# Optimization experiments

Measured on AMD Instinct MI355X. Metric: run time of the kernel, lower is better.

## Reference

```python
import jax, jax.numpy as jnp
import numpy as np

N = 50000
E = 800000
D_IN = 128
D_HID = 512
D_OUT = 128
BN_EPS = 1e-5


def setup_inputs() -> dict:
    key = jax.random.key(0)
    ks = jax.random.split(key, 12)
    inp = {}
    inp["v"] = jax.random.normal(ks[0], (N, D_IN), dtype=jnp.float32)
    inp["src"] = jax.random.randint(ks[1], (E,), 0, N, dtype=jnp.int32)
    inp["dst"] = jax.random.randint(ks[2], (E,), 0, N, dtype=jnp.int32)
    inp["edge_weight"] = jax.random.uniform(ks[3], (E,), dtype=jnp.float32)
    # learned parameters
    inp["epsilon"] = jnp.zeros((1, 1), dtype=jnp.float32)  # nn.Parameter([[0.0]])
    s1 = 1.0 / np.sqrt(D_IN)
    s2 = 1.0 / np.sqrt(D_HID)
    inp["W1"] = jax.random.uniform(ks[4], (D_IN, D_HID), minval=-s1, maxval=s1, dtype=jnp.float32)
    inp["b1"] = jax.random.uniform(ks[5], (D_HID,), minval=-s1, maxval=s1, dtype=jnp.float32)
    inp["gamma1"] = jnp.ones((D_HID,), dtype=jnp.float32)
    inp["beta1"] = jnp.zeros((D_HID,), dtype=jnp.float32)
    inp["W2"] = jax.random.uniform(ks[6], (D_HID, D_OUT), minval=-s2, maxval=s2, dtype=jnp.float32)
    inp["b2"] = jax.random.uniform(ks[7], (D_OUT,), minval=-s2, maxval=s2, dtype=jnp.float32)
    inp["gamma2"] = jnp.ones((D_OUT,), dtype=jnp.float32)
    inp["beta2"] = jnp.zeros((D_OUT,), dtype=jnp.float32)
    return inp


def _batchnorm(x, gamma, beta):
    # training-mode BN: batch mean / biased variance over the node axis
    mean = jnp.mean(x, axis=0)
    var = jnp.mean(jnp.square(x - mean), axis=0)
    return gamma * (x - mean) * jax.lax.rsqrt(var + BN_EPS) + beta


def reference(v, src, dst, edge_weight, epsilon, W1, b1, gamma1, beta1, W2, b2, gamma2, beta2):
    n = v.shape[0]
    # sparse.mm(a, v): out[dst] += w * v[src]
    msgs = v[src] * edge_weight[:, None]               # [E, D_IN]
    v_agg = jax.ops.segment_sum(msgs, dst, num_segments=n)  # [N, D_IN]
    v_agg = v_agg + epsilon * v                        # epsilon residual
    h = jax.nn.relu(_batchnorm(v_agg @ W1 + b1, gamma1, beta1))
    out = jax.nn.relu(_batchnorm(h @ W2 + b2, gamma2, beta2))
    return out
```

## Files before the change

kernel.cpp:

```cpp
#include <hip/hip_runtime.h>

#define N_NODES 50000
#define E_EDGES 800000
#define D_INF   128
#define D_HIDF  512
#define D_OUTF  128
#define SCAN_NB ((N_NODES + 255) / 256)
#define M1BLKS  ((N_NODES + 255) / 256)
#define FBLKS   ((N_NODES + 63) / 64)
#define EQ      (E_EDGES / 4)

#define CAST_NB  3125
#define PREPW_NB 256
#define HIST_NB  ((EQ + 255) / 256)
#define PREP_ALL_NB (CAST_NB + 2 * PREPW_NB + HIST_NB)

typedef unsigned short u16;
typedef __attribute__((ext_vector_type(8))) short short8;
typedef __attribute__((ext_vector_type(4))) float floatx4;
typedef const __attribute__((address_space(1))) void gas_t;
typedef __attribute__((address_space(3))) void las_t;

__device__ __forceinline__ u16 f2bf(float f) {
    union { float f; unsigned u; } v; v.f = f;
    unsigned r = (v.u + 0x7fffu + ((v.u >> 16) & 1u)) >> 16;
    return (u16)r;
}
__device__ __forceinline__ float bf2f(u16 b) {
    union { unsigned u; float f; } v; v.u = ((unsigned)b) << 16; return v.f;
}

__global__ __launch_bounds__(256) void prep_all_kernel(
        const float* __restrict__ v, const float* __restrict__ W1,
        const float* __restrict__ W2, const int* __restrict__ dst,
        u16* __restrict__ vbf, u16* __restrict__ W1t, u16* __restrict__ W2t,
        int* __restrict__ counts, int* __restrict__ pos) {
    int b = blockIdx.x;
    int tid = threadIdx.x;
    if (b < CAST_NB) {
        int i = b * 256 + tid;
        const float4 a = ((const float4*)v)[i * 2];
        const float4 c = ((const float4*)v)[i * 2 + 1];
        u16 o[8];
        o[0] = f2bf(a.x); o[1] = f2bf(a.y); o[2] = f2bf(a.z); o[3] = f2bf(a.w);
        o[4] = f2bf(c.x); o[5] = f2bf(c.y); o[6] = f2bf(c.z); o[7] = f2bf(c.w);
        ((float4*)vbf)[i] = *(const float4*)o;
    } else if (b < CAST_NB + PREPW_NB) {
        int idx = (b - CAST_NB) * 256 + tid;
        int k1 = idx >> 9, n1 = idx & 511;
        W1t[n1 * 128 + k1] = f2bf(W1[idx]);
    } else if (b < CAST_NB + 2 * PREPW_NB) {
        int idx = (b - CAST_NB - PREPW_NB) * 256 + tid;
        int k2 = idx >> 7, n2 = idx & 127;
        W2t[n2 * 512 + k2] = f2bf(W2[idx]);
    } else {
        int t = (b - CAST_NB - 2 * PREPW_NB) * 256 + tid;
        if (t >= EQ) return;
        int d0 = dst[t];
        int d1 = dst[t + EQ];
        int d2 = dst[t + 2 * EQ];
        int d3 = dst[t + 3 * EQ];
        int p0 = atomicAdd(&counts[d0], 1);
        int p1 = atomicAdd(&counts[d1], 1);
        int p2 = atomicAdd(&counts[d2], 1);
        int p3 = atomicAdd(&counts[d3], 1);
        pos[t]          = p0;
        pos[t + EQ]     = p1;
        pos[t + 2 * EQ] = p2;
        pos[t + 3 * EQ] = p3;
    }
}

__global__ __launch_bounds__(256) void reduce_kernel(const int* __restrict__ counts,
                                                     int* __restrict__ block_sums) {
    __shared__ int lsum[4];
    int tid = threadIdx.x;
    int gid = blockIdx.x * 256 + tid;
    int s = (gid < N_NODES) ? counts[gid] : 0;
#pragma unroll
    for (int off = 32; off; off >>= 1) s += __shfl_down(s, off);
    if ((tid & 63) == 0) lsum[tid >> 6] = s;
    __syncthreads();
    if (tid == 0) block_sums[blockIdx.x] = lsum[0] + lsum[1] + lsum[2] + lsum[3];
}

__global__ __launch_bounds__(256) void scan_final(const int* __restrict__ counts,
                                                  const int* __restrict__ block_sums,
                                                  int* __restrict__ row_start) {
    __shared__ int sh[256];
    __shared__ int bs[256];
    int tid = threadIdx.x;
    int gid = blockIdx.x * 256 + tid;
    sh[tid] = (gid < N_NODES) ? counts[gid] : 0;
    bs[tid] = (tid < SCAN_NB) ? block_sums[tid] : 0;
    __syncthreads();
    for (int off = 1; off < 256; off <<= 1) {
        int t1 = (tid >= off) ? sh[tid - off] : 0;
        int t2 = (tid >= off) ? bs[tid - off] : 0;
        __syncthreads();
        sh[tid] += t1;
        bs[tid] += t2;
        __syncthreads();
    }
    int boff = (blockIdx.x == 0) ? 0 : bs[blockIdx.x - 1];
    int excl = (tid == 0) ? 0 : sh[tid - 1];
    if (gid < N_NODES) row_start[gid] = boff + excl;
    if (gid == 0) row_start[N_NODES] = E_EDGES;
}

__global__ void fill_kernel(const int* __restrict__ src, const int* __restrict__ dst,
                            const float* __restrict__ w, const int* __restrict__ pos,
                            const int* __restrict__ row_start,
                            int2* __restrict__ csr_ew) {
    int e = blockIdx.x * blockDim.x + threadIdx.x;
    if (e >= E_EDGES) return;
    int d = dst[e];
    int idx = row_start[d] + pos[e];
    int2 rec;
    rec.x = src[e];
    rec.y = __float_as_int(w[e]);
    csr_ew[idx] = rec;
}

__global__ __launch_bounds__(256) void gather_kernel(const u16* __restrict__ vbf,
                                                     const int* __restrict__ row_start,
                                                     const int2* __restrict__ csr_ew,
                                                     const float* __restrict__ eps_p,
                                                     u16* __restrict__ vagg) {
    int node = blockIdx.x * 16 + (threadIdx.x >> 4);
    if (node >= N_NODES) return;
    int c8 = (threadIdx.x & 15) << 3;
    int beg = row_start[node];
    int end = row_start[node + 1];
    float a[8] = {};
    int j = beg;
    for (; j + 1 < end; j += 2) {
        int2 e0 = csr_ew[j];
        int2 e1 = csr_ew[j + 1];
        float w0 = __int_as_float(e0.y);
        float w1 = __int_as_float(e1.y);
        float4 r0 = *(const float4*)(vbf + (size_t)e0.x * D_INF + c8);
        float4 r1 = *(const float4*)(vbf + (size_t)e1.x * D_INF + c8);
        const u16* p0 = (const u16*)&r0;
        const u16* p1 = (const u16*)&r1;
#pragma unroll
        for (int t = 0; t < 8; ++t) a[t] += w0 * bf2f(p0[t]);
#pragma unroll
        for (int t = 0; t < 8; ++t) a[t] += w1 * bf2f(p1[t]);
    }
    if (j < end) {
        int2 e0 = csr_ew[j];
        float w0 = __int_as_float(e0.y);
        float4 r0 = *(const float4*)(vbf + (size_t)e0.x * D_INF + c8);
        const u16* p0 = (const u16*)&r0;
#pragma unroll
        for (int t = 0; t < 8; ++t) a[t] += w0 * bf2f(p0[t]);
    }
    float e = eps_p[0];
    float4 rn = *(const float4*)(vbf + (size_t)node * D_INF + c8);
    const u16* pn = (const u16*)&rn;
    u16 o[8];
#pragma unroll
    for (int t = 0; t < 8; ++t) o[t] = f2bf(a[t] + e * bf2f(pn[t]));
    *(float4*)(vagg + (size_t)node * D_INF + c8) = *(const float4*)o;
}

__global__ __launch_bounds__(512) void stats_gemm1(
        const u16* __restrict__ A, const u16* __restrict__ Bt,
        const float* __restrict__ bias,
        float* __restrict__ psum, float* __restrict__ psq, int M) {
    __shared__ __align__(16) char smem[24576];
    u16* As = (u16*)smem;
    u16* Bs = (u16*)(smem + 16384);
    const int bm = blockIdx.y * 256;
    const int bn = blockIdx.x * 128;
    const int tid = threadIdx.x;
    const int wave = tid >> 6, lane = tid & 63;
    const int wr = wave >> 1, wc = wave & 1;
    const int wm = wr * 64, wn = wc * 64;
    const int lm = lane & 15, quad = lane >> 4;
    floatx4 acc[4][4] = {};
    for (int ks = 0; ks < 4; ++ks) {
        const int k0 = ks << 5;
        {
            const int sub = lane >> 2, s = lane & 3;
#pragma unroll
            for (int t = 0; t < 3; ++t) {
                int ch = wave * 3 + t;
                if (ch < 16) {
                    int row = ch * 16 + sub;
                    int grow = bm + row; if (grow > M - 1) grow = M - 1;
                    int ss = s ^ (row & 3);
                    __builtin_amdgcn_global_load_lds(
                        (gas_t*)(A + (size_t)grow * 128 + k0 + ss * 8),
                        (las_t*)(As + row * 32 + s * 8), 16, 0, 0);
                } else {
                    int row = (ch - 16) * 16 + sub;
                    int ss = s ^ (row & 3);
                    __builtin_amdgcn_global_load_lds(
                        (gas_t*)(Bt + (size_t)(bn + row) * 128 + k0 + ss * 8),
                        (las_t*)(Bs + row * 32 + s * 8), 16, 0, 0);
                }
            }
        }
        __syncthreads();
        short8 af[4], bfr[4];
#pragma unroll
        for (int i = 0; i < 4; ++i) {
            int row = wm + i * 16 + lm;
            af[i] = *(const short8*)&As[row * 32 + ((quad ^ (row & 3)) * 8)];
        }
#pragma unroll
        for (int j = 0; j < 4; ++j) {
            int row = wn + j * 16 + lm;
            bfr[j] = *(const short8*)&Bs[row * 32 + ((quad ^ (row & 3)) * 8)];
        }
#pragma unroll
        for (int i = 0; i < 4; ++i)
#pragma unroll
            for (int j = 0; j < 4; ++j)
                acc[i][j] = __builtin_amdgcn_mfma_f32_16x16x32_bf16(af[i], bfr[j], acc[i][j], 0, 0, 0);
        __syncthreads();
    }
    float* redS = (float*)smem;
    float* redQ = redS + 128;
    if (tid < 128) { redS[tid] = 0.f; redQ[tid] = 0.f; }
    __syncthreads();
#pragma unroll
    for (int j = 0; j < 4; ++j) {
        int cl = wn + j * 16 + lm;
        float bj = bias[bn + cl];
        float s = 0.f, q = 0.f;
#pragma unroll
        for (int i = 0; i < 4; ++i) {
            int row0 = bm + wm + i * 16 + quad * 4;
#pragma unroll
            for (int r = 0; r < 4; ++r)
                if (row0 + r < M) { float x = acc[i][j][r] + bj; s += x; q += x * x; }
        }
        s += __shfl_xor(s, 16); q += __shfl_xor(q, 16);
        s += __shfl_xor(s, 32); q += __shfl_xor(q, 32);
        if (quad == 0) { atomicAdd(&redS[cl], s); atomicAdd(&redQ[cl], q); }
    }
    __syncthreads();
    if (tid < 128) {
        psum[(size_t)blockIdx.y * 512 + bn + tid] = redS[tid];
        psq [(size_t)blockIdx.y * 512 + bn + tid] = redQ[tid];
    }
}

__global__ __launch_bounds__(512, 4) void fused_mlp(
        const u16* __restrict__ vagg, const u16* __restrict__ W1t,
        const u16* __restrict__ W2t,
        const float* __restrict__ b1, const float* __restrict__ scale1,
        const float* __restrict__ shift1, const float* __restrict__ b2,
        u16* __restrict__ x2, float* __restrict__ psum, float* __restrict__ psq,
        int M) {
    __shared__ __align__(16) char smem[81920];
    u16* As  = (u16*)smem;
    u16* W1s = (u16*)(smem + 16384);
    u16* W2s = (u16*)smem;
    u16* hs  = (u16*)(smem + 16384);
    const int bm = blockIdx.x * 64;
    const int tid = threadIdx.x;
    const int wave = tid >> 6, lane = tid & 63;
    const int wr = wave >> 2, wc = wave & 3;
    const int wm = wr * 32;
    const int wn1 = wc * 128;
    const int wn2 = wc * 32;
    const int lm = lane & 15, quad = lane >> 4;

    floatx4 acc1[2][8] = {};
    floatx4 acc2[2][2] = {};

    auto stage_w1 = [&](int win) {
#pragma unroll
        for (int u = 0; u < 8; ++u) {
            int c = tid + u * 512;
            int col = c >> 3, s = c & 7;
            __builtin_amdgcn_global_load_lds(
                (gas_t*)(W1t + (size_t)col * 128 + win * 64 + ((s ^ (col & 7)) * 8)),
                (las_t*)(W1s + col * 64 + s * 8), 16, 0, 0);
        }
    };
    auto stage_w2 = [&](int win) {
#pragma unroll
        for (int u = 0; u < 2; ++u) {
            int c = tid + u * 512;
            int n = c >> 3, s = c & 7;
            __builtin_amdgcn_global_load_lds(
                (gas_t*)(W2t + (size_t)n * 512 + win * 64 + ((s ^ (n & 7)) * 8)),
                (las_t*)(W2s + n * 64 + s * 8), 16, 0, 0);
        }
    };
    auto compute1 = [&](int ks) {
        short8 a[2], b[8];
#pragma unroll
        for (int i = 0; i < 2; ++i) {
            int row = wm + i * 16 + lm;
            a[i] = *(const short8*)&As[row * 128 + (((ks * 4 + quad) ^ (row & 7)) * 8)];
        }
#pragma unroll
        for (int j = 0; j < 8; ++j) {
            int col = wn1 + j * 16 + lm;
            b[j] = *(const short8*)&W1s[col * 64 + ((((ks & 1) * 4 + quad) ^ (col & 7)) * 8)];
        }
#pragma unroll
        for (int i = 0; i < 2; ++i)
#pragma unroll
            for (int j = 0; j < 8; ++j)
                acc1[i][j] = __builtin_amdgcn_mfma_f32_16x16x32_bf16(a[i], b[j], acc1[i][j], 0, 0, 0);
    };
    auto compute2 = [&](int ks) {
        short8 a[2], b[2];
#pragma unroll
        for (int i = 0; i < 2; ++i) {
            int row = wm + i * 16 + lm;
            a[i] = *(const short8*)&hs[row * 512 + (((ks * 4 + quad) ^ (row & 7)) * 8)];
        }
#pragma unroll
        for (int j = 0; j < 2; ++j) {
            int n = wn2 + j * 16 + lm;
            b[j] = *(const short8*)&W2s[n * 64 + ((((ks & 1) * 4 + quad) ^ (n & 7)) * 8)];
        }
#pragma unroll
        for (int i = 0; i < 2; ++i)
#pragma unroll
            for (int j = 0; j < 2; ++j)
                acc2[i][j] = __builtin_amdgcn_mfma_f32_16x16x32_bf16(a[i], b[j], acc2[i][j], 0, 0, 0);
    };

#pragma unroll
    for (int u = 0; u < 2; ++u) {
        int c = tid + u * 512;
        int row = c >> 4, s = c & 15;
        int grow = bm + row; if (grow > M - 1) grow = M - 1;
        __builtin_amdgcn_global_load_lds(
            (gas_t*)(vagg + (size_t)grow * 128 + ((s ^ (row & 7)) * 8)),
            (las_t*)(As + row * 128 + s * 8), 16, 0, 0);
    }
    stage_w1(0);
    __syncthreads();
    compute1(0); compute1(1);
    __syncthreads();
    stage_w1(1);
    __syncthreads();
    compute1(2); compute1(3);
    __syncthreads();

    stage_w2(0);
    {
        float hsc[8], hsh[8];
#pragma unroll
        for (int j = 0; j < 8; ++j) {
            int col = wn1 + j * 16 + lm;
            float sc = scale1[col];
            hsc[j] = sc;
            hsh[j] = shift1[col] + sc * b1[col];
        }
#pragma unroll
        for (int i = 0; i < 2; ++i)
#pragma unroll
            for (int j = 0; j < 8; ++j)
#pragma unroll
                for (int r = 0; r < 4; ++r) {
                    int row = wm + i * 16 + quad * 4 + r;
                    int col = wn1 + j * 16 + lm;
                    float hv = fmaxf(0.f, acc1[i][j][r] * hsc[j] + hsh[j]);
                    hs[row * 512 + (((col >> 3) ^ (row & 7)) * 8) + (col & 7)] = f2bf(hv);
                }
    }
    __syncthreads();

#pragma unroll
    for (int win = 0; win < 8; ++win) {
        compute2(win * 2); compute2(win * 2 + 1);
        __syncthreads();
        if (win < 7) { stage_w2(win + 1); __syncthreads(); }
    }

    float* redS = (float*)smem;
    float* redQ = redS + 128;
    if (tid < 128) { redS[tid] = 0.f; redQ[tid] = 0.f; }
    __syncthreads();
    float bj2[2];
#pragma unroll
    for (int j = 0; j < 2; ++j) {
        int cl = wn2 + j * 16 + lm;
        bj2[j] = b2[cl];
        float s = 0.f, q = 0.f;
#pragma unroll
        for (int i = 0; i < 2; ++i) {
            int row0 = bm + wm + i * 16 + quad * 4;
#pragma unroll
            for (int r = 0; r < 4; ++r)
                if (row0 + r < M) { float x = acc2[i][j][r] + bj2[j]; s += x; q += x * x; }
        }
        s += __shfl_xor(s, 16); q += __shfl_xor(q, 16);
        s += __shfl_xor(s, 32); q += __shfl_xor(q, 32);
        if (quad == 0) { atomicAdd(&redS[cl], s); atomicAdd(&redQ[cl], q); }
    }
    __syncthreads();
    if (tid < 128) {
        psum[(size_t)blockIdx.x * 128 + tid] = redS[tid];
        psq [(size_t)blockIdx.x * 128 + tid] = redQ[tid];
    }
    __syncthreads();

    float* obuf = (float*)smem;
#pragma unroll
    for (int i = 0; i < 2; ++i)
#pragma unroll
        for (int j = 0; j < 2; ++j)
#pragma unroll
            for (int r = 0; r < 4; ++r) {
                int row = wm + i * 16 + quad * 4 + r;
                int col = wn2 + j * 16 + lm;
                obuf[row * 132 + col] = acc2[i][j][r] + bj2[j];
            }
    __syncthreads();
    {
        int row = tid >> 3, seg = (tid & 7) * 16;
        int grow = bm + row;
        if (grow < M) {
            u16 ob[16];
#pragma unroll
            for (int t = 0; t < 4; ++t) {
                float4 f = *(float4*)&obuf[row * 132 + seg + t * 4];
                ob[t * 4 + 0] = f2bf(f.x);
                ob[t * 4 + 1] = f2bf(f.y);
                ob[t * 4 + 2] = f2bf(f.z);
                ob[t * 4 + 3] = f2bf(f.w);
            }
            u16* dp = x2 + (size_t)grow * 128 + seg;
            *(float4*)dp       = *(float4*)ob;
            *(float4*)(dp + 8) = *(float4*)(ob + 8);
        }
    }
}

__global__ __launch_bounds__(1024) void bn_finalize_kernel(
        const float* __restrict__ psum, const float* __restrict__ psq,
        const float* __restrict__ gamma, const float* __restrict__ beta,
        float* __restrict__ scale, float* __restrict__ shift,
        int nblocks, int Ncols, float inv_n) {
    __shared__ float shS[16][64];
    __shared__ float shQ[16][64];
    const int tx = threadIdx.x;
    const int ty = threadIdx.y;
    const int c = blockIdx.x * 64 + tx;
    float s = 0.f, q = 0.f;
    for (int b = ty; b < nblocks; b += 16) {
        s += psum[(size_t)b * Ncols + c];
        q += psq [(size_t)b * Ncols + c];
    }
    shS[ty][tx] = s;
    shQ[ty][tx] = q;
    __syncthreads();
    if (ty == 0) {
        float S = 0.f, Q = 0.f;
#pragma unroll
        for (int r = 0; r < 16; ++r) { S += shS[r][tx]; Q += shQ[r][tx]; }
        float m = S * inv_n;
        float var = Q * inv_n - m * m;
        float rs = rsqrtf(var + 1e-5f);
        float sc = gamma[c] * rs;
        scale[c] = sc;
        shift[c] = beta[c] - sc * m;
    }
}

__global__ void bn2_apply_kernel(const u16* __restrict__ X, float* __restrict__ Y,
                                 const float* __restrict__ scale,
                                 const float* __restrict__ shift, int n8) {
    int i = blockIdx.x * blockDim.x + threadIdx.x;
    if (i >= n8) return;
    int c = (i & 15) << 3;
    float4 raw = ((const float4*)X)[i];
    const u16* xb = (const u16*)&raw;
    float4 sc0 = *(const float4*)(scale + c);
    float4 sc1 = *(const float4*)(scale + c + 4);
    float4 sh0 = *(const float4*)(shift + c);
    float4 sh1 = *(const float4*)(shift + c + 4);
    float4 y0, y1;
    y0.x = fmaxf(0.f, bf2f(xb[0]) * sc0.x + sh0.x);
    y0.y = fmaxf(0.f, bf2f(xb[1]) * sc0.y + sh0.y);
    y0.z = fmaxf(0.f, bf2f(xb[2]) * sc0.z + sh0.z);
    y0.w = fmaxf(0.f, bf2f(xb[3]) * sc0.w + sh0.w);
    y1.x = fmaxf(0.f, bf2f(xb[4]) * sc1.x + sh1.x);
    y1.y = fmaxf(0.f, bf2f(xb[5]) * sc1.y + sh1.y);
    y1.z = fmaxf(0.f, bf2f(xb[6]) * sc1.z + sh1.z);
    y1.w = fmaxf(0.f, bf2f(xb[7]) * sc1.w + sh1.w);
    ((float4*)Y)[i * 2]     = y0;
    ((float4*)Y)[i * 2 + 1] = y1;
}

extern "C" void kernel_launch(void* const* d_in, const int* in_sizes, int n_in,
                              void* d_out, int out_size, void* d_ws, size_t ws_size,
                              hipStream_t stream) {
    const float* v    = (const float*)d_in[0];
    const int* src    = (const int*)d_in[1];
    const int* dst    = (const int*)d_in[2];
    const float* ew   = (const float*)d_in[3];
    const float* eps  = (const float*)d_in[4];
    const float* W1   = (const float*)d_in[5];
    const float* b1   = (const float*)d_in[6];
    const float* g1   = (const float*)d_in[7];
    const float* be1  = (const float*)d_in[8];
    const float* W2   = (const float*)d_in[9];
    const float* b2   = (const float*)d_in[10];
    const float* g2   = (const float*)d_in[11];
    const float* be2  = (const float*)d_in[12];
    float* out = (float*)d_out;

    char* base = (char*)d_ws;
    u16* vbf  = (u16*)(base + 51200000ull);
    u16* vagg = (u16*)(base + 64000000ull);
    u16* x2   = (u16*)(base + 76800000ull);
    u16* W1t  = (u16*)(base + 89600000ull);
    u16* W2t  = (u16*)(base + 89731072ull);
    float* psum   = (float*)(base + 89862144ull);
    float* psq    = (float*)(base + 90663168ull);
    float* scale1 = (float*)(base + 91464192ull);
    float* shift1 = scale1 + 512;
    float* scale2 = shift1 + 512;
    float* shift2 = scale2 + 128;
    int* counts     = (int*)(shift2 + 128);
    int* row_start  = counts + 50000;
    int* pos        = row_start + 50004;
    int2* csr_ew    = (int2*)(pos + 800000);
    int* block_sums = (int*)(csr_ew + 800000);

    hipMemsetAsync(counts, 0, (size_t)50000 * sizeof(int), stream);

    prep_all_kernel<<<PREP_ALL_NB, 256, 0, stream>>>(v, W1, W2, dst, vbf, W1t, W2t,
                                                     counts, pos);
    reduce_kernel<<<SCAN_NB, 256, 0, stream>>>(counts, block_sums);
    scan_final<<<SCAN_NB, 256, 0, stream>>>(counts, block_sums, row_start);
    fill_kernel<<<(E_EDGES + 255) / 256, 256, 0, stream>>>(src, dst, ew, pos, row_start, csr_ew);
    gather_kernel<<<(N_NODES + 15) / 16, 256, 0, stream>>>(vbf, row_start, csr_ew, eps, vagg);

    {
        dim3 grid(D_HIDF / 128, M1BLKS);
        stats_gemm1<<<grid, 512, 0, stream>>>(vagg, W1t, b1, psum, psq, N_NODES);
    }
    bn_finalize_kernel<<<D_HIDF / 64, dim3(64, 16), 0, stream>>>(
        psum, psq, g1, be1, scale1, shift1, M1BLKS, D_HIDF, 1.0f / N_NODES);

    fused_mlp<<<FBLKS, 512, 0, stream>>>(vagg, W1t, W2t, b1, scale1, shift1, b2,
                                         x2, psum, psq, N_NODES);
    bn_finalize_kernel<<<D_OUTF / 64, dim3(64, 16), 0, stream>>>(
        psum, psq, g2, be2, scale2, shift2, FBLKS, D_OUTF, 1.0f / N_NODES);

    {
        int n8 = N_NODES * D_OUTF / 8;
        bn2_apply_kernel<<<(n8 + 255) / 256, 256, 0, stream>>>(x2, out, scale2, shift2, n8);
    }
}
```

Before: 275.4 us.

## Retile BN1 stats GEMM to full-width rows and widen histogram and gather unrolls

Replaces the 256x128-tiled stats GEMM with a 64-row block kernel that computes all 512 hidden columns per block, mirroring fused_mlp's tiling. A-tile loads are shared across all columns, and partial-stat buffers are placed in dead CSR scratch (pos/csr_ew). The histogram part of the prep kernel now handles 8 edges per thread and runs first, and the gather loop unrolls by 4 edges to keep more loads in flight. This trades more per-block partial sums for BN finalize (782 vs 196 rows) and higher register pressure for better reuse and memory-level parallelism.

```diff
diff --git a/kernel.cpp b/kernel.cpp
--- a/kernel.cpp
+++ b/kernel.cpp
@@ -6,14 +6,13 @@
 #define D_HIDF  512
 #define D_OUTF  128
 #define SCAN_NB ((N_NODES + 255) / 256)
-#define M1BLKS  ((N_NODES + 255) / 256)
 #define FBLKS   ((N_NODES + 63) / 64)
-#define EQ      (E_EDGES / 4)
-
+#define EQ8     (E_EDGES / 8)
+
+#define HIST_NB  ((EQ8 + 255) / 256)
 #define CAST_NB  3125
 #define PREPW_NB 256
-#define HIST_NB  ((EQ + 255) / 256)
-#define PREP_ALL_NB (CAST_NB + 2 * PREPW_NB + HIST_NB)
+#define PREP_ALL_NB (HIST_NB + CAST_NB + 2 * PREPW_NB)
 
 typedef unsigned short u16;
 typedef __attribute__((ext_vector_type(8))) short short8;
@@ -37,37 +36,32 @@
         int* __restrict__ counts, int* __restrict__ pos) {
     int b = blockIdx.x;
     int tid = threadIdx.x;
-    if (b < CAST_NB) {
-        int i = b * 256 + tid;
+    if (b < HIST_NB) {
+        int t = b * 256 + tid;
+        if (t >= EQ8) return;
+        int d[8], p[8];
+#pragma unroll
+        for (int k = 0; k < 8; ++k) d[k] = dst[t + k * EQ8];
+#pragma unroll
+        for (int k = 0; k < 8; ++k) p[k] = atomicAdd(&counts[d[k]], 1);
+#pragma unroll
+        for (int k = 0; k < 8; ++k) pos[t + k * EQ8] = p[k];
+    } else if (b < HIST_NB + CAST_NB) {
+        int i = (b - HIST_NB) * 256 + tid;
         const float4 a = ((const float4*)v)[i * 2];
         const float4 c = ((const float4*)v)[i * 2 + 1];
         u16 o[8];
         o[0] = f2bf(a.x); o[1] = f2bf(a.y); o[2] = f2bf(a.z); o[3] = f2bf(a.w);
         o[4] = f2bf(c.x); o[5] = f2bf(c.y); o[6] = f2bf(c.z); o[7] = f2bf(c.w);
         ((float4*)vbf)[i] = *(const float4*)o;
-    } else if (b < CAST_NB + PREPW_NB) {
-        int idx = (b - CAST_NB) * 256 + tid;
+    } else if (b < HIST_NB + CAST_NB + PREPW_NB) {
+        int idx = (b - HIST_NB - CAST_NB) * 256 + tid;
         int k1 = idx >> 9, n1 = idx & 511;
         W1t[n1 * 128 + k1] = f2bf(W1[idx]);
-    } else if (b < CAST_NB + 2 * PREPW_NB) {
-        int idx = (b - CAST_NB - PREPW_NB) * 256 + tid;
+    } else {
+        int idx = (b - HIST_NB - CAST_NB - PREPW_NB) * 256 + tid;
         int k2 = idx >> 7, n2 = idx & 127;
         W2t[n2 * 512 + k2] = f2bf(W2[idx]);
-    } else {
-        int t = (b - CAST_NB - 2 * PREPW_NB) * 256 + tid;
-        if (t >= EQ) return;
-        int d0 = dst[t];
-        int d1 = dst[t + EQ];
-        int d2 = dst[t + 2 * EQ];
-        int d3 = dst[t + 3 * EQ];
-        int p0 = atomicAdd(&counts[d0], 1);
-        int p1 = atomicAdd(&counts[d1], 1);
-        int p2 = atomicAdd(&counts[d2], 1);
-        int p3 = atomicAdd(&counts[d3], 1);
-        pos[t]          = p0;
-        pos[t + EQ]     = p1;
-        pos[t + 2 * EQ] = p2;
-        pos[t + 3 * EQ] = p3;
     }
 }
 
@@ -134,21 +128,33 @@
     int end = row_start[node + 1];
     float a[8] = {};
     int j = beg;
-    for (; j + 1 < end; j += 2) {
+    for (; j + 3 < end; j += 4) {
         int2 e0 = csr_ew[j];
         int2 e1 = csr_ew[j + 1];
+        int2 e2 = csr_ew[j + 2];
+        int2 e3 = csr_ew[j + 3];
         float w0 = __int_as_float(e0.y);
         float w1 = __int_as_float(e1.y);
+        float w2 = __int_as_float(e2.y);
+        float w3 = __int_as_float(e3.y);
         float4 r0 = *(const float4*)(vbf + (size_t)e0.x * D_INF + c8);
         float4 r1 = *(const float4*)(vbf + (size_t)e1.x * D_INF + c8);
+        float4 r2 = *(const float4*)(vbf + (size_t)e2.x * D_INF + c8);
+        float4 r3 = *(const float4*)(vbf + (size_t)e3.x * D_INF + c8);
         const u16* p0 = (const u16*)&r0;
         const u16* p1 = (const u16*)&r1;
+        const u16* p2 = (const u16*)&r2;
+        const u16* p3 = (const u16*)&r3;
 #pragma unroll
         for (int t = 0; t < 8; ++t) a[t] += w0 * bf2f(p0[t]);
 #pragma unroll
         for (int t = 0; t < 8; ++t) a[t] += w1 * bf2f(p1[t]);
-    }
-    if (j < end) {
+#pragma unroll
+        for (int t = 0; t < 8; ++t) a[t] += w2 * bf2f(p2[t]);
+#pragma unroll
+        for (int t = 0; t < 8; ++t) a[t] += w3 * bf2f(p3[t]);
+    }
+    for (; j < end; ++j) {
         int2 e0 = csr_ew[j];
         float w0 = __int_as_float(e0.y);
         float4 r0 = *(const float4*)(vbf + (size_t)e0.x * D_INF + c8);
@@ -165,88 +171,93 @@
     *(float4*)(vagg + (size_t)node * D_INF + c8) = *(const float4*)o;
 }
 
-__global__ __launch_bounds__(512) void stats_gemm1(
-        const u16* __restrict__ A, const u16* __restrict__ Bt,
-        const float* __restrict__ bias,
+__global__ __launch_bounds__(512, 4) void stats_mlp1(
+        const u16* __restrict__ vagg, const u16* __restrict__ W1t,
+        const float* __restrict__ b1,
         float* __restrict__ psum, float* __restrict__ psq, int M) {
-    __shared__ __align__(16) char smem[24576];
-    u16* As = (u16*)smem;
-    u16* Bs = (u16*)(smem + 16384);
-    const int bm = blockIdx.y * 256;
-    const int bn = blockIdx.x * 128;
+    __shared__ __align__(16) char smem[81920];
+    u16* As  = (u16*)smem;
+    u16* W1s = (u16*)(smem + 16384);
+    const int bm = blockIdx.x * 64;
     const int tid = threadIdx.x;
     const int wave = tid >> 6, lane = tid & 63;
-    const int wr = wave >> 1, wc = wave & 1;
-    const int wm = wr * 64, wn = wc * 64;
+    const int wr = wave >> 2, wc = wave & 3;
+    const int wm = wr * 32;
+    const int wn1 = wc * 128;
     const int lm = lane & 15, quad = lane >> 4;
-    floatx4 acc[4][4] = {};
-    for (int ks = 0; ks < 4; ++ks) {
-        const int k0 = ks << 5;
-        {
-            const int sub = lane >> 2, s = lane & 3;
-#pragma unroll
-            for (int t = 0; t < 3; ++t) {
-                int ch = wave * 3 + t;
-                if (ch < 16) {
-                    int row = ch * 16 + sub;
-                    int grow = bm + row; if (grow > M - 1) grow = M - 1;
-                    int ss = s ^ (row & 3);
-                    __builtin_amdgcn_global_load_lds(
-                        (gas_t*)(A + (size_t)grow * 128 + k0 + ss * 8),
-                        (las_t*)(As + row * 32 + s * 8), 16, 0, 0);
-                } else {
-                    int row = (ch - 16) * 16 + sub;
-                    int ss = s ^ (row & 3);
-                    __builtin_amdgcn_global_load_lds(
-                        (gas_t*)(Bt + (size_t)(bn + row) * 128 + k0 + ss * 8),
-                        (las_t*)(Bs + row * 32 + s * 8), 16, 0, 0);
-                }
-            }
-        }
-        __syncthreads();
-        short8 af[4], bfr[4];
-#pragma unroll
-        for (int i = 0; i < 4; ++i) {
+
+    floatx4 acc1[2][8] = {};
+
+    auto stage_w1 = [&](int win) {
+#pragma unroll
+        for (int u = 0; u < 8; ++u) {
+            int c = tid + u * 512;
+            int col = c >> 3, s = c & 7;
+            __builtin_amdgcn_global_load_lds(
+                (gas_t*)(W1t + (size_t)col * 128 + win * 64 + ((s ^ (col & 7)) * 8)),
+                (las_t*)(W1s + col * 64 + s * 8), 16, 0, 0);
+        }
+    };
+    auto compute1 = [&](int ks) {
+        short8 a[2], b[8];
+#pragma unroll
+        for (int i = 0; i < 2; ++i) {
             int row = wm + i * 16 + lm;
-            af[i] = *(const short8*)&As[row * 32 + ((quad ^ (row & 3)) * 8)];
-        }
-#pragma unroll
-        for (int j = 0; j < 4; ++j) {
-            int row = wn + j * 16 + lm;
-            bfr[j] = *(const short8*)&Bs[row * 32 + ((quad ^ (row & 3)) * 8)];
-        }
-#pragma unroll
-        for (int i = 0; i < 4; ++i)
-#pragma unroll
-            for (int j = 0; j < 4; ++j)
-                acc[i][j] = __builtin_amdgcn_mfma_f32_16x16x32_bf16(af[i], bfr[j], acc[i][j], 0, 0, 0);
-        __syncthreads();
-    }
+            a[i] = *(const short8*)&As[row * 128 + (((ks * 4 + quad) ^ (row & 7)) * 8)];
+        }
+#pragma unroll
+        for (int j = 0; j < 8; ++j) {
+            int col = wn1 + j * 16 + lm;
+            b[j] = *(const short8*)&W1s[col * 64 + ((((ks & 1) * 4 + quad) ^ (col & 7)) * 8)];
+        }
+#pragma unroll
+        for (int i = 0; i < 2; ++i)
+#pragma unroll
+            for (int j = 0; j < 8; ++j)
+                acc1[i][j] = __builtin_amdgcn_mfma_f32_16x16x32_bf16(a[i], b[j], acc1[i][j], 0, 0, 0);
+    };
+
+#pragma unroll
+    for (int u = 0; u < 2; ++u) {
+        int c = tid + u * 512;
+        int row = c >> 4, s = c & 15;
+        int grow = bm + row; if (grow > M - 1) grow = M - 1;
+        __builtin_amdgcn_global_load_lds(
+            (gas_t*)(vagg + (size_t)grow * 128 + ((s ^ (row & 7)) * 8)),
+            (las_t*)(As + row * 128 + s * 8), 16, 0, 0);
+    }
+    stage_w1(0);
+    __syncthreads();
+    compute1(0); compute1(1);
+    __syncthreads();
+    stage_w1(1);
+    __syncthreads();
+    compute1(2); compute1(3);
+    __syncthreads();
+
     float* redS = (float*)smem;
-    float* redQ = redS + 128;
-    if (tid < 128) { redS[tid] = 0.f; redQ[tid] = 0.f; }
-    __syncthreads();
-#pragma unroll
-    for (int j = 0; j < 4; ++j) {
-        int cl = wn + j * 16 + lm;
-        float bj = bias[bn + cl];
+    float* redQ = redS + 512;
+    redS[tid] = 0.f; redQ[tid] = 0.f;
+    __syncthreads();
+#pragma unroll
+    for (int j = 0; j < 8; ++j) {
+        int cl = wn1 + j * 16 + lm;
+        float bj = b1[cl];
         float s = 0.f, q = 0.f;
 #pragma unroll
-        for (int i = 0; i < 4; ++i) {
+        for (int i = 0; i < 2; ++i) {
             int row0 = bm + wm + i * 16 + quad * 4;
 #pragma unroll
             for (int r = 0; r < 4; ++r)
-                if (row0 + r < M) { float x = acc[i][j][r] + bj; s += x; q += x * x; }
+                if (row0 + r < M) { float x = acc1[i][j][r] + bj; s += x; q += x * x; }
         }
         s += __shfl_xor(s, 16); q += __shfl_xor(q, 16);
         s += __shfl_xor(s, 32); q += __shfl_xor(q, 32);
         if (quad == 0) { atomicAdd(&redS[cl], s); atomicAdd(&redQ[cl], q); }
     }
     __syncthreads();
-    if (tid < 128) {
-        psum[(size_t)blockIdx.y * 512 + bn + tid] = redS[tid];
-        psq [(size_t)blockIdx.y * 512 + bn + tid] = redQ[tid];
-    }
+    psum[(size_t)blockIdx.x * 512 + tid] = redS[tid];
+    psq [(size_t)blockIdx.x * 512 + tid] = redQ[tid];
 }
 
 __global__ __launch_bounds__(512, 4) void fused_mlp(
@@ -519,8 +530,8 @@
     u16* x2   = (u16*)(base + 76800000ull);
     u16* W1t  = (u16*)(base + 89600000ull);
     u16* W2t  = (u16*)(base + 89731072ull);
-    float* psum   = (float*)(base + 89862144ull);
-    float* psq    = (float*)(base + 90663168ull);
+    float* psum2  = (float*)(base + 89862144ull);
+    float* psq2   = (float*)(base + 90663168ull);
     float* scale1 = (float*)(base + 91464192ull);
     float* shift1 = scale1 + 512;
     float* scale2 = shift1 + 512;
@@ -530,6 +541,8 @@
     int* pos        = row_start + 50004;
     int2* csr_ew    = (int2*)(pos + 800000);
     int* block_sums = (int*)(csr_ew + 800000);
+    float* psum1 = (float*)pos;
+    float* psq1  = (float*)csr_ew;
 
     hipMemsetAsync(counts, 0, (size_t)50000 * sizeof(int), stream);
 
@@ -540,17 +553,14 @@
     fill_kernel<<<(E_EDGES + 255) / 256, 256, 0, stream>>>(src, dst, ew, pos, row_start, csr_ew);
     gather_kernel<<<(N_NODES + 15) / 16, 256, 0, stream>>>(vbf, row_start, csr_ew, eps, vagg);
 
-    {
-        dim3 grid(D_HIDF / 128, M1BLKS);
-        stats_gemm1<<<grid, 512, 0, stream>>>(vagg, W1t, b1, psum, psq, N_NODES);
-    }
+    stats_mlp1<<<FBLKS, 512, 0, stream>>>(vagg, W1t, b1, psum1, psq1, N_NODES);
     bn_finalize_kernel<<<D_HIDF / 64, dim3(64, 16), 0, stream>>>(
-        psum, psq, g1, be1, scale1, shift1, M1BLKS, D_HIDF, 1.0f / N_NODES);
+        psum1, psq1, g1, be1, scale1, shift1, FBLKS, D_HIDF, 1.0f / N_NODES);
 
     fused_mlp<<<FBLKS, 512, 0, stream>>>(vagg, W1t, W2t, b1, scale1, shift1, b2,
-                                         x2, psum, psq, N_NODES);
+                                         x2, psum2, psq2, N_NODES);
     bn_finalize_kernel<<<D_OUTF / 64, dim3(64, 16), 0, stream>>>(
-        psum, psq, g2, be2, scale2, shift2, FBLKS, D_OUTF, 1.0f / N_NODES);
+        psum2, psq2, g2, be2, scale2, shift2, FBLKS, D_OUTF, 1.0f / N_NODES);
 
     {
         int n8 = N_NODES * D_OUTF / 8;
```

After: 291.1 us. 5.7% more time.
